# Kernel optimization log

Hardware: AMD Instinct MI355X
Metric: run time of the kernel (lower is better)

The kernel has to match this reference:

```python
import jax, jax.numpy as jnp
import numpy as np

QBITS = 8  # fake-quant bit width from q_config
DT_RANK = 128
D_STATE = 16


def fake_quant_tensor(x, bits=QBITS):
    """Per-tensor symmetric fake quantization (quantize-dequantize) with STE."""
    qmax = 2.0 ** (bits - 1) - 1.0
    s = jnp.maximum(jnp.max(jnp.abs(x)) / qmax, 1e-8)
    q = jnp.clip(jnp.round(x / s), -qmax - 1.0, qmax) * s
    return x + jax.lax.stop_gradient(q - x)


def fake_quant_per_channel(w, bits=QBITS):
    """Per-output-channel symmetric fake quantization for weights [out, in]."""
    qmax = 2.0 ** (bits - 1) - 1.0
    s = jnp.maximum(jnp.max(jnp.abs(w), axis=-1, keepdims=True) / qmax, 1e-8)
    q = jnp.clip(jnp.round(w / s), -qmax - 1.0, qmax) * s
    return w + jax.lax.stop_gradient(q - w)


def setup_inputs() -> dict:
    key = jax.random.key(0)
    ks = jax.random.split(key, 8)
    B, L, D_MODEL = 2, 4096, 2048
    d_inner = D_MODEL  # expand = 1.0
    x = jax.random.normal(ks[0], (B, L, D_MODEL), jnp.float32)
    prompt = 0.1 * jax.random.normal(ks[1], (B, L, D_STATE), jnp.float32)
    # x_proj: Linear(d_inner -> dt_rank + 2*d_state), no bias
    Wx = jax.random.normal(ks[2], (DT_RANK + 2 * D_STATE, d_inner), jnp.float32) / np.sqrt(d_inner)
    # dt_proj: Linear(dt_rank -> d_inner), with bias
    Wdt = jax.random.normal(ks[3], (d_inner, DT_RANK), jnp.float32) / np.sqrt(DT_RANK)
    bdt = 0.1 * jax.random.normal(ks[4], (d_inner,), jnp.float32)
    # S4D-real init for A_log, D skip param (standard Mamba selective-scan params)
    A_log = jnp.log(jnp.tile(jnp.arange(1, D_STATE + 1, dtype=jnp.float32), (d_inner, 1)))
    Dskip = jax.random.normal(ks[5], (d_inner,), jnp.float32)
    return dict(x=x, prompt=prompt, Wx=Wx, Wdt=Wdt, bdt=bdt, A_log=A_log, Dskip=Dskip)


def reference(x, prompt, Wx, Wdt, bdt, A_log, Dskip):
    # x_proj with fake-quantized weight, then split into dt / B / C
    x_dbl = jnp.einsum('bld,od->blo', x, fake_quant_per_channel(Wx))
    dts = x_dbl[..., :DT_RANK]
    Bs = x_dbl[..., DT_RANK:DT_RANK + D_STATE]
    Cs = x_dbl[..., DT_RANK + D_STATE:]
    # dt_proj with fake-quantized weight
    dts = jnp.einsum('blr,or->blo', dts, fake_quant_per_channel(Wdt)) + bdt
    # activation fake-quant of scan inputs
    u_q = fake_quant_tensor(x)          # [B, L, d_inner]
    dt_q = fake_quant_tensor(dts)       # [B, L, d_inner]
    B_q = fake_quant_tensor(Bs)         # [B, L, d_state]
    C_q = fake_quant_tensor(Cs + prompt)  # [B, L, d_state]
    # selective scan (quantized SSM weights A, D)
    A = -jnp.exp(fake_quant_per_channel(A_log))  # [d_inner, d_state]
    D_q = fake_quant_tensor(Dskip)               # [d_inner]
    dt = jax.nn.softplus(dt_q)

    def step(h, inp):
        u_t, dt_t, B_t, C_t = inp  # [B,d], [B,d], [B,n], [B,n]
        dA = jnp.exp(dt_t[:, :, None] * A)             # [B, d, n]
        dBu = (dt_t * u_t)[:, :, None] * B_t[:, None, :]
        h = dA * h + dBu                               # [B, d, n]
        y = jnp.einsum('bdn,bn->bd', h, C_t)
        return h, y

    Bsz, L, d = x.shape
    h0 = jnp.zeros((Bsz, d, D_STATE), x.dtype)
    xs = (jnp.swapaxes(u_q, 0, 1), jnp.swapaxes(dt, 0, 1),
          jnp.swapaxes(B_q, 0, 1), jnp.swapaxes(C_q, 0, 1))
    _, ys = jax.lax.scan(step, h0, xs)  # ys: [L, B, d]
    return jnp.swapaxes(ys, 0, 1) + u_q * D_q
```

## Files before the change

### kernel.cpp

```cpp
#include <hip/hip_runtime.h>
#include <hip/hip_bf16.h>

#define BSZ    2
#define LSEQ   4096
#define DMODEL 2048
#define DTR    128
#define DST    16
#define ODIM   160
#define MROWS  (BSZ*LSEQ)
#define CH     64
#define TT     (LSEQ/CH)
#define STRD   258
#define LOG2E  1.44269504088896340736f
#define LN2    0.69314718055994530942f

typedef short  short8  __attribute__((ext_vector_type(8)));
typedef float  floatx4 __attribute__((ext_vector_type(4)));
typedef float  floatx2 __attribute__((ext_vector_type(2)));

__device__ __forceinline__ unsigned short f2bf(float f) {
    unsigned u = __float_as_uint(f);
    u += 0x7fffu + ((u >> 16) & 1u);
    return (unsigned short)(u >> 16);
}
__device__ __forceinline__ float quantv(float x, float s, float inv_s) {
    float q = rintf(x * inv_s);
    q = fminf(fmaxf(q, -128.0f), 127.0f);
    return q * s;
}
__device__ __forceinline__ float softplus_fast(float v) {
    float t = __builtin_amdgcn_exp2f(-fabsf(v) * LOG2E);
    return fmaxf(v, 0.0f) + LN2 * __log2f(1.0f + t);
}
__device__ __forceinline__ float scale_from_bits(unsigned bits) {
    return fmaxf(__uint_as_float(bits) * (1.0f/127.0f), 1e-8f);
}
__device__ __forceinline__ int pidx(int r, int k, int K) {
    return (r >> 4)*(16*K) + ((k >> 5) << 9) + (((r & 15) + (((k & 31) >> 3) << 4)) << 3) + (k & 7);
}

#define PB_WX  160
#define PB_WDT 128
#define PB_A   128
#define PB_D   1
#define PREP_BLOCKS (PB_WX + PB_WDT + PB_A + PB_D)

__global__ __launch_bounds__(256) void k_prep(
    const float* __restrict__ Wx, const float* __restrict__ Wdt,
    const float* __restrict__ A_log, const float* __restrict__ Dskip,
    unsigned short* __restrict__ Wxq, unsigned short* __restrict__ Wdtq,
    float* __restrict__ a2, float* __restrict__ Dq)
{
    int bid = blockIdx.x, tid = threadIdx.x;
    __shared__ float red[256];
    if (bid < PB_WX) {
        int o = bid, base = o * DMODEL;
        float m = 0.0f;
        for (int i = tid; i < DMODEL; i += 256) m = fmaxf(m, fabsf(Wx[base+i]));
        red[tid] = m; __syncthreads();
        for (int s2 = 128; s2 > 0; s2 >>= 1) { if (tid < s2) red[tid] = fmaxf(red[tid], red[tid+s2]); __syncthreads(); }
        float s = fmaxf(red[0]*(1.0f/127.0f), 1e-8f), inv = 1.0f/s;
        for (int i = tid; i < DMODEL; i += 256)
            Wxq[pidx(o, i, DMODEL)] = f2bf(quantv(Wx[base+i], s, inv));
    } else if (bid < PB_WX + PB_WDT) {
        int n = (bid - PB_WX)*16 + (tid >> 4);
        int k0 = (tid & 15)*8;
        const float* src = Wdt + (size_t)n*DTR + k0;
        float4 v0 = *reinterpret_cast<const float4*>(src);
        float4 v1 = *reinterpret_cast<const float4*>(src + 4);
        float m = fmaxf(fmaxf(fmaxf(fabsf(v0.x), fabsf(v0.y)), fmaxf(fabsf(v0.z), fabsf(v0.w))),
                        fmaxf(fmaxf(fabsf(v1.x), fabsf(v1.y)), fmaxf(fabsf(v1.z), fabsf(v1.w))));
        for (int off = 1; off < 16; off <<= 1) m = fmaxf(m, __shfl_xor(m, off, 16));
        float s = fmaxf(m*(1.0f/127.0f), 1e-8f), inv = 1.0f/s;
        short8 o8;
        o8[0]=(short)f2bf(quantv(v0.x,s,inv)); o8[1]=(short)f2bf(quantv(v0.y,s,inv));
        o8[2]=(short)f2bf(quantv(v0.z,s,inv)); o8[3]=(short)f2bf(quantv(v0.w,s,inv));
        o8[4]=(short)f2bf(quantv(v1.x,s,inv)); o8[5]=(short)f2bf(quantv(v1.y,s,inv));
        o8[6]=(short)f2bf(quantv(v1.z,s,inv)); o8[7]=(short)f2bf(quantv(v1.w,s,inv));
        *reinterpret_cast<short8*>(Wdtq + pidx(n, k0, DTR)) = o8;
    } else if (bid < PB_WX + PB_WDT + PB_A) {
        int d = (bid - PB_WX - PB_WDT)*16 + (tid >> 4);
        int n = tid & 15;
        float v = A_log[d*DST + n];
        float m = fabsf(v);
        for (int off = 1; off < 16; off <<= 1) m = fmaxf(m, __shfl_xor(m, off, 16));
        float s = fmaxf(m*(1.0f/127.0f), 1e-8f);
        float q = quantv(v, s, 1.0f/s);
        a2[d*DST + n] = -expf(q) * LOG2E;
    } else {
        float m = 0.0f;
        for (int i = tid; i < DMODEL; i += 256) m = fmaxf(m, fabsf(Dskip[i]));
        red[tid] = m; __syncthreads();
        for (int s2 = 128; s2 > 0; s2 >>= 1) { if (tid < s2) red[tid] = fmaxf(red[tid], red[tid+s2]); __syncthreads(); }
        float s = fmaxf(red[0]*(1.0f/127.0f), 1e-8f), inv = 1.0f/s;
        for (int i = tid; i < DMODEL; i += 256) Dq[i] = quantv(Dskip[i], s, inv);
    }
}

__global__ __launch_bounds__(256) void k_mm1(
    const float* __restrict__ x, const unsigned short* __restrict__ Wxq,
    const unsigned short* __restrict__ Wdtq, const float* __restrict__ bdt,
    const float* __restrict__ prompt,
    unsigned short* __restrict__ xdblbf, float* __restrict__ xbc,
    unsigned* __restrict__ scales)
{
    int tid = threadIdx.x, w = tid >> 6, lane = tid & 63;
    int mrow = lane & 15, quad = lane >> 4;
    int mt = blockIdx.x, m0 = mt*16, k0 = w*512;
    floatx4 acc[10] = {};
    float xmax = 0.0f;
    const float* arow = x + (size_t)(m0 + mrow)*DMODEL + k0 + quad*8;
    for (int kk = 0; kk < 512; kk += 32) {
        const float4* ap = reinterpret_cast<const float4*>(arow + kk);
        float4 a0 = ap[0], a1 = ap[1];
        xmax = fmaxf(xmax, fmaxf(fmaxf(fabsf(a0.x), fabsf(a0.y)), fmaxf(fabsf(a0.z), fabsf(a0.w))));
        xmax = fmaxf(xmax, fmaxf(fmaxf(fabsf(a1.x), fabsf(a1.y)), fmaxf(fabsf(a1.z), fabsf(a1.w))));
        short8 af;
        af[0]=(short)f2bf(a0.x); af[1]=(short)f2bf(a0.y); af[2]=(short)f2bf(a0.z); af[3]=(short)f2bf(a0.w);
        af[4]=(short)f2bf(a1.x); af[5]=(short)f2bf(a1.y); af[6]=(short)f2bf(a1.z); af[7]=(short)f2bf(a1.w);
        int kcidx = (k0 + kk) >> 5;
        #pragma unroll
        for (int j = 0; j < 10; ++j) {
            short8 bf = *reinterpret_cast<const short8*>(Wxq + j*16*DMODEL + kcidx*512 + lane*8);
            acc[j] = __builtin_amdgcn_mfma_f32_16x16x32_bf16(af, bf, acc[j], 0, 0, 0);
        }
    }
    for (int off = 32; off; off >>= 1) xmax = fmaxf(xmax, __shfl_xor(xmax, off, 64));
    __shared__ float red[4*2560];
    __shared__ float redB[256], redC[256];
    __shared__ float wred[4], wd[4];
    __shared__ unsigned short lds_abf[2048];
    if (lane == 0) wred[w] = xmax;
    #pragma unroll
    for (int j = 0; j < 10; ++j) {
        float4 v = make_float4(acc[j][0], acc[j][1], acc[j][2], acc[j][3]);
        *reinterpret_cast<float4*>(&red[w*2560 + (j*16 + mrow)*16 + quad*4]) = v;
    }
    __syncthreads();
    float bmax = 0.0f, cmax = 0.0f;
    #pragma unroll
    for (int j = 0; j < 10; ++j) {
        int e = j*256 + tid;
        float v = red[e] + red[2560+e] + red[5120+e] + red[7680+e];
        int col = e >> 4, rowin = e & 15, row = m0 + rowin;
        if (col < DTR) {
            int off = ((col>>5)<<9) + ((rowin + (((col&31)>>3)<<4))<<3) + (col&7);
            unsigned short bfb = f2bf(v);
            xdblbf[mt*16*DTR + off] = bfb;
            lds_abf[off] = bfb;
        } else if (col < DTR + DST) {
            bmax = fmaxf(bmax, fabsf(v));
            xbc[(size_t)row*32 + (col - DTR)] = v;
        } else {
            v += prompt[(size_t)row*DST + (col - DTR - DST)];
            cmax = fmaxf(cmax, fabsf(v));
            xbc[(size_t)row*32 + 16 + (col - DTR - DST)] = v;
        }
    }
    redB[tid] = bmax; redC[tid] = cmax; __syncthreads();
    for (int s2 = 128; s2 > 0; s2 >>= 1) {
        if (tid < s2) { redB[tid] = fmaxf(redB[tid], redB[tid+s2]); redC[tid] = fmaxf(redC[tid], redC[tid+s2]); }
        __syncthreads();
    }
    short8 afr[4];
    #pragma unroll
    for (int kc = 0; kc < 4; ++kc)
        afr[kc] = *reinterpret_cast<const short8*>(lds_abf + (kc<<9) + lane*8);
    float dmax = 0.0f;
    for (int jj = 0; jj < 32; ++jj) {
        int ntile = w*32 + jj;
        const unsigned short* bb = Wdtq + (size_t)ntile*16*DTR + lane*8;
        floatx4 acc2 = {};
        #pragma unroll
        for (int kc = 0; kc < 4; ++kc) {
            short8 bf = *reinterpret_cast<const short8*>(bb + (kc<<9));
            acc2 = __builtin_amdgcn_mfma_f32_16x16x32_bf16(afr[kc], bf, acc2, 0, 0, 0);
        }
        float bv = bdt[ntile*16 + mrow];
        #pragma unroll
        for (int r = 0; r < 4; ++r) dmax = fmaxf(dmax, fabsf(acc2[r] + bv));
    }
    for (int off = 32; off; off >>= 1) dmax = fmaxf(dmax, __shfl_xor(dmax, off, 64));
    if (lane == 0) wd[w] = dmax;
    __syncthreads();
    if (tid == 0) {
        atomicMax(&scales[0], __float_as_uint(fmaxf(fmaxf(wred[0], wred[1]), fmaxf(wred[2], wred[3]))));
        atomicMax(&scales[1], __float_as_uint(redB[0]));
        atomicMax(&scales[2], __float_as_uint(redC[0]));
        atomicMax(&scales[3], __float_as_uint(fmaxf(fmaxf(wd[0], wd[1]), fmaxf(wd[2], wd[3]))));
    }
}

__global__ __launch_bounds__(256) void k_scan1(
    const unsigned short* __restrict__ Ap, const unsigned short* __restrict__ Bp,
    const float* __restrict__ bdt, const float* __restrict__ x,
    const float* __restrict__ xbc, const float* __restrict__ a2,
    const unsigned* __restrict__ scales, unsigned* __restrict__ u8g,
    float* __restrict__ Aprod, float* __restrict__ hfin)
{
    int bid = blockIdx.x, tid = threadIdx.x;
    int w = tid >> 6, lane = tid & 63;
    int mrow = lane & 15, quad = lane >> 4;
    int b = bid >> 9, rem = bid & 511, dblk = rem >> 6, ch = rem & 63;
    int d0 = dblk*256, t0 = ch*TT;
    int d = d0 + tid;
    float s_u  = scale_from_bits(scales[0]), inv_su = 1.0f/s_u;
    float s_B  = scale_from_bits(scales[1]), inv_sB  = 1.0f/s_B;
    float s_dt = scale_from_bits(scales[3]), inv_sdt = 1.0f/s_dt;
    floatx2 a22[8];
    {
        const floatx2* ap = reinterpret_cast<const floatx2*>(a2 + (size_t)d*DST);
        #pragma unroll
        for (int i = 0; i < 8; ++i) a22[i] = ap[i];
    }
    floatx2 h2[8];
    #pragma unroll
    for (int i = 0; i < 8; ++i) h2[i] = (floatx2){0.0f, 0.0f};
    float sdt = 0.0f;
    __shared__ float lds_dts[16*STRD];
    __shared__ unsigned lds_u[16*64];
    __shared__ __align__(16) float Bq_p[16*16];
    for (int st = 0; st < TT/16; ++st) {
        int tb = t0 + st*16;
        int gm = (b*LSEQ + tb) >> 4;
        short8 afr[4];
        #pragma unroll
        for (int kc = 0; kc < 4; ++kc)
            afr[kc] = *reinterpret_cast<const short8*>(Ap + (size_t)gm*16*DTR + (kc<<9) + lane*8);
        #pragma unroll
        for (int j = 0; j < 4; ++j) {
            int ntile = dblk*16 + w*4 + j;
            int dloc = w*64 + j*16 + mrow;
            float bdtv = bdt[d0 + dloc];
            floatx4 acc = {};
            #pragma unroll
            for (int kc = 0; kc < 4; ++kc) {
                short8 bf = *reinterpret_cast<const short8*>(Bp + (size_t)ntile*16*DTR + (kc<<9) + lane*8);
                acc = __builtin_amdgcn_mfma_f32_16x16x32_bf16(afr[kc], bf, acc, 0, 0, 0);
            }
            #pragma unroll
            for (int r = 0; r < 4; ++r)
                lds_dts[(quad*4 + r)*STRD + dloc] = acc[r] + bdtv;
        }
        {
            const float4* x4 = reinterpret_cast<const float4*>(x);
            #pragma unroll
            for (int i = 0; i < 4; ++i) {
                int q = i*256 + tid, row = q >> 6, c4 = q & 63;
                size_t gi = (size_t)(b*LSEQ + tb + row)*(DMODEL/4) + dblk*64 + c4;
                float4 v = x4[gi];
                int q0 = (int)fminf(fmaxf(rintf(v.x*inv_su), -128.0f), 127.0f);
                int q1 = (int)fminf(fmaxf(rintf(v.y*inv_su), -128.0f), 127.0f);
                int q2 = (int)fminf(fmaxf(rintf(v.z*inv_su), -128.0f), 127.0f);
                int q3 = (int)fminf(fmaxf(rintf(v.w*inv_su), -128.0f), 127.0f);
                unsigned u = (q0 & 255) | ((q1 & 255) << 8) | ((q2 & 255) << 16) | ((unsigned)(q3 & 255) << 24);
                lds_u[row*64 + c4] = u;
                u8g[gi] = u;
            }
            Bq_p[tid] = quantv(xbc[(size_t)(b*LSEQ + tb + (tid>>4))*32 + (tid&15)], s_B, inv_sB);
        }
        __syncthreads();
        const signed char* lub = reinterpret_cast<const signed char*>(lds_u);
        for (int t = 0; t < 16; ++t) {
            float dtq = quantv(lds_dts[t*STRD + tid], s_dt, inv_sdt);
            float dtv = softplus_fast(dtq);
            float uq  = s_u * (float)lub[t*256 + tid];
            float dtu = dtv * uq;
            sdt += dtv;
            floatx2 dtv2 = {dtv, dtv}, dtu2 = {dtu, dtu};
            const floatx2* bq2 = reinterpret_cast<const floatx2*>(&Bq_p[t*16]);
            #pragma unroll
            for (int n2 = 0; n2 < 8; ++n2) {
                floatx2 e = a22[n2] * dtv2;
                floatx2 dA; dA.x = __builtin_amdgcn_exp2f(e.x); dA.y = __builtin_amdgcn_exp2f(e.y);
                h2[n2] = dA*h2[n2] + bq2[n2]*dtu2;
            }
        }
        __syncthreads();
    }
    size_t ob = ((size_t)((b*CH + ch)*DMODEL + d))*DST;
    floatx2 sdt2 = {sdt, sdt};
    #pragma unroll
    for (int i = 0; i < 4; ++i) {
        floatx2 e0 = a22[2*i] * sdt2, e1 = a22[2*i+1] * sdt2;
        float4 av = make_float4(__builtin_amdgcn_exp2f(e0.x), __builtin_amdgcn_exp2f(e0.y),
                                __builtin_amdgcn_exp2f(e1.x), __builtin_amdgcn_exp2f(e1.y));
        float4 hv = make_float4(h2[2*i].x, h2[2*i].y, h2[2*i+1].x, h2[2*i+1].y);
        *reinterpret_cast<float4*>(Aprod + ob + 4*i) = av;
        *reinterpret_cast<float4*>(hfin  + ob + 4*i) = hv;
    }
}

__global__ __launch_bounds__(256) void k_mid(
    float* __restrict__ Aprod, const float* __restrict__ hfin)
{
    int f = blockIdx.x*256 + threadIdx.x;
    int b = f >> 15, dn = f & 32767;
    size_t base = (size_t)b*CH*32768 + dn;
    float h = 0.0f;
    #pragma unroll 4
    for (int ch = 0; ch < CH; ++ch) {
        size_t o = base + (size_t)ch*32768;
        float a = Aprod[o], hf = hfin[o];
        Aprod[o] = h;
        h = fmaf(a, h, hf);
    }
}

__global__ __launch_bounds__(256) void k_scan3(
    const unsigned short* __restrict__ Ap, const unsigned short* __restrict__ Bp,
    const float* __restrict__ bdt, const unsigned* __restrict__ u8g,
    const float* __restrict__ xbc, const float* __restrict__ a2,
    const float* __restrict__ Dq, const unsigned* __restrict__ scales,
    const float* __restrict__ hinit, float* __restrict__ out)
{
    int bid = blockIdx.x, tid = threadIdx.x;
    int w = tid >> 6, lane = tid & 63;
    int mrow = lane & 15, quad = lane >> 4;
    int b = bid >> 9, rem = bid & 511, dblk = rem >> 6, ch = rem & 63;
    int d0 = dblk*256, t0 = ch*TT;
    int d = d0 + tid;
    float s_u  = scale_from_bits(scales[0]);
    float s_B  = scale_from_bits(scales[1]), inv_sB  = 1.0f/s_B;
    float s_C  = scale_from_bits(scales[2]), inv_sC  = 1.0f/s_C;
    float s_dt = scale_from_bits(scales[3]), inv_sdt = 1.0f/s_dt;
    float dqd = Dq[d];
    floatx2 a22[8];
    {
        const floatx2* ap = reinterpret_cast<const floatx2*>(a2 + (size_t)d*DST);
        #pragma unroll
        for (int i = 0; i < 8; ++i) a22[i] = ap[i];
    }
    size_t ob = ((size_t)((b*CH + ch)*DMODEL + d))*DST;
    floatx2 h2[8];
    #pragma unroll
    for (int i = 0; i < 4; ++i) {
        float4 hv = *reinterpret_cast<const float4*>(hinit + ob + 4*i);
        h2[2*i]   = (floatx2){hv.x, hv.y};
        h2[2*i+1] = (floatx2){hv.z, hv.w};
    }
    __shared__ float lds_dts[16*STRD];
    __shared__ unsigned lds_u[16*64];
    __shared__ __align__(16) float Bq_p[16*16];
    __shared__ __align__(16) float Cq_p[16*16];
    for (int st = 0; st < TT/16; ++st) {
        int tb = t0 + st*16;
        int gm = (b*LSEQ + tb) >> 4;
        short8 afr[4];
        #pragma unroll
        for (int kc = 0; kc < 4; ++kc)
            afr[kc] = *reinterpret_cast<const short8*>(Ap + (size_t)gm*16*DTR + (kc<<9) + lane*8);
        #pragma unroll
        for (int j = 0; j < 4; ++j) {
            int ntile = dblk*16 + w*4 + j;
            int dloc = w*64 + j*16 + mrow;
            float bdtv = bdt[d0 + dloc];
            floatx4 acc = {};
            #pragma unroll
            for (int kc = 0; kc < 4; ++kc) {
                short8 bf = *reinterpret_cast<const short8*>(Bp + (size_t)ntile*16*DTR + (kc<<9) + lane*8);
                acc = __builtin_amdgcn_mfma_f32_16x16x32_bf16(afr[kc], bf, acc, 0, 0, 0);
            }
            #pragma unroll
            for (int r = 0; r < 4; ++r)
                lds_dts[(quad*4 + r)*STRD + dloc] = acc[r] + bdtv;
        }
        {
            #pragma unroll
            for (int i = 0; i < 4; ++i) {
                int q = i*256 + tid, row = q >> 6, c4 = q & 63;
                size_t gi = (size_t)(b*LSEQ + tb + row)*(DMODEL/4) + dblk*64 + c4;
                lds_u[row*64 + c4] = u8g[gi];
            }
            size_t px = (size_t)(b*LSEQ + tb + (tid>>4))*32;
            Bq_p[tid] = quantv(xbc[px + (tid&15)],      s_B, inv_sB);
            Cq_p[tid] = quantv(xbc[px + 16 + (tid&15)], s_C, inv_sC);
        }
        __syncthreads();
        const signed char* lub = reinterpret_cast<const signed char*>(lds_u);
        for (int t = 0; t < 16; ++t) {
            float dtq = quantv(lds_dts[t*STRD + tid], s_dt, inv_sdt);
            float dtv = softplus_fast(dtq);
            float uq  = s_u * (float)lub[t*256 + tid];
            float dtu = dtv * uq;
            floatx2 dtv2 = {dtv, dtv}, dtu2 = {dtu, dtu};
            const floatx2* bq2 = reinterpret_cast<const floatx2*>(&Bq_p[t*16]);
            const floatx2* cq2 = reinterpret_cast<const floatx2*>(&Cq_p[t*16]);
            floatx2 y2 = {0.0f, 0.0f};
            #pragma unroll
            for (int n2 = 0; n2 < 8; ++n2) {
                floatx2 e = a22[n2] * dtv2;
                floatx2 dA; dA.x = __builtin_amdgcn_exp2f(e.x); dA.y = __builtin_amdgcn_exp2f(e.y);
                h2[n2] = dA*h2[n2] + bq2[n2]*dtu2;
                y2 = y2 + h2[n2]*cq2[n2];
            }
            float y = y2.x + y2.y;
            __builtin_nontemporal_store(y + uq * dqd, out + (size_t)(b*LSEQ + tb + t)*DMODEL + d);
        }
        __syncthreads();
    }
}

extern "C" void kernel_launch(void* const* d_in, const int* in_sizes, int n_in,
                              void* d_out, int out_size, void* d_ws, size_t ws_size,
                              hipStream_t stream)
{
    const float* x      = (const float*)d_in[0];
    const float* prompt = (const float*)d_in[1];
    const float* Wx     = (const float*)d_in[2];
    const float* Wdt    = (const float*)d_in[3];
    const float* bdt    = (const float*)d_in[4];
    const float* A_log  = (const float*)d_in[5];
    const float* Dskip  = (const float*)d_in[6];
    float* out = (float*)d_out;
    char* ws = (char*)d_ws;
    size_t off = 0;
    unsigned* scales       = (unsigned*)(ws + off);        off += 256;
    unsigned short* Wxq    = (unsigned short*)(ws + off);  off += (size_t)ODIM*DMODEL*2;
    unsigned short* Wdtq   = (unsigned short*)(ws + off);  off += (size_t)DMODEL*DTR*2;
    float* a2              = (float*)(ws + off);           off += (size_t)DMODEL*DST*4;
    float* Dq              = (float*)(ws + off);           off += (size_t)DMODEL*4;
    float* xbc             = (float*)(ws + off);           off += (size_t)MROWS*32*4;
    unsigned short* xdblbf = (unsigned short*)(ws + off);  off += (size_t)MROWS*DTR*2;
    unsigned* u8g          = (unsigned*)(ws + off);        off += (size_t)MROWS*DMODEL;
    float* Aprod           = (float*)(ws + off);           off += (size_t)BSZ*CH*DMODEL*DST*4;
    float* hfin            = (float*)(ws + off);           off += (size_t)BSZ*CH*DMODEL*DST*4;

    hipMemsetAsync(scales, 0, 256, stream);
    hipLaunchKernelGGL(k_prep, dim3(PREP_BLOCKS), dim3(256), 0, stream,
                       Wx, Wdt, A_log, Dskip, Wxq, Wdtq, a2, Dq);
    hipLaunchKernelGGL(k_mm1, dim3(MROWS/16), dim3(256), 0, stream,
                       x, Wxq, Wdtq, bdt, prompt, xdblbf, xbc, scales);
    hipLaunchKernelGGL(k_scan1, dim3(BSZ*8*CH), dim3(256), 0, stream,
                       xdblbf, Wdtq, bdt, x, xbc, a2, scales, u8g, Aprod, hfin);
    hipLaunchKernelGGL(k_mid, dim3(BSZ*DMODEL*DST/256), dim3(256), 0, stream,
                       Aprod, hfin);
    hipLaunchKernelGGL(k_scan3, dim3(BSZ*8*CH), dim3(256), 0, stream,
                       xdblbf, Wdtq, bdt, u8g, xbc, a2, Dq, scales, Aprod, out);
}
```

Baseline: 328.3 us.

## Store int8 dt codes in scan1, reuse in scan3, double-buffer LDS stages

k_scan1 now quantizes the dt projection to int8 codes and writes them to global memory, so k_scan3 reads them back instead of redoing the dt_proj MFMA matmul. Both scan kernels move to 128-thread blocks with twice as many blocks, and they double-buffer the LDS staging so loads for the next 16-step tile are issued before the current tile's recurrence runs, with one barrier per stage. This removes duplicated matmul work and a barrier per stage. The cost is an extra 16 MB write and read of dt codes and smaller blocks that now stage less data each.

```diff
diff --git a/kernel.cpp b/kernel.cpp
--- a/kernel.cpp
+++ b/kernel.cpp
@@ -10,7 +10,6 @@
 #define MROWS  (BSZ*LSEQ)
 #define CH     64
 #define TT     (LSEQ/CH)
-#define STRD   258
 #define LOG2E  1.44269504088896340736f
 #define LN2    0.69314718055994530942f
 
@@ -27,6 +26,9 @@
     float q = rintf(x * inv_s);
     q = fminf(fmaxf(q, -128.0f), 127.0f);
     return q * s;
+}
+__device__ __forceinline__ int qcode(float x, float inv_s) {
+    return (int)fminf(fmaxf(rintf(x * inv_s), -128.0f), 127.0f);
 }
 __device__ __forceinline__ float softplus_fast(float v) {
     float t = __builtin_amdgcn_exp2f(-fabsf(v) * LOG2E);
@@ -191,18 +193,19 @@
     }
 }
 
-__global__ __launch_bounds__(256) void k_scan1(
+__global__ __launch_bounds__(128) void k_scan1(
     const unsigned short* __restrict__ Ap, const unsigned short* __restrict__ Bp,
     const float* __restrict__ bdt, const float* __restrict__ x,
     const float* __restrict__ xbc, const float* __restrict__ a2,
-    const unsigned* __restrict__ scales, unsigned* __restrict__ u8g,
+    const unsigned* __restrict__ scales,
+    unsigned* __restrict__ u8g, signed char* __restrict__ dt8g,
     float* __restrict__ Aprod, float* __restrict__ hfin)
 {
     int bid = blockIdx.x, tid = threadIdx.x;
     int w = tid >> 6, lane = tid & 63;
     int mrow = lane & 15, quad = lane >> 4;
-    int b = bid >> 9, rem = bid & 511, dblk = rem >> 6, ch = rem & 63;
-    int d0 = dblk*256, t0 = ch*TT;
+    int b = bid >> 10, rem = bid & 1023, dblk = rem >> 6, ch = rem & 63;
+    int d0 = dblk*128, t0 = ch*TT;
     int d = d0 + tid;
     float s_u  = scale_from_bits(scales[0]), inv_su = 1.0f/s_u;
     float s_B  = scale_from_bits(scales[1]), inv_sB  = 1.0f/s_B;
@@ -217,66 +220,75 @@
     #pragma unroll
     for (int i = 0; i < 8; ++i) h2[i] = (floatx2){0.0f, 0.0f};
     float sdt = 0.0f;
-    __shared__ float lds_dts[16*STRD];
-    __shared__ unsigned lds_u[16*64];
-    __shared__ __align__(16) float Bq_p[16*16];
-    for (int st = 0; st < TT/16; ++st) {
-        int tb = t0 + st*16;
-        int gm = (b*LSEQ + tb) >> 4;
-        short8 afr[4];
-        #pragma unroll
-        for (int kc = 0; kc < 4; ++kc)
-            afr[kc] = *reinterpret_cast<const short8*>(Ap + (size_t)gm*16*DTR + (kc<<9) + lane*8);
-        #pragma unroll
-        for (int j = 0; j < 4; ++j) {
-            int ntile = dblk*16 + w*4 + j;
-            int dloc = w*64 + j*16 + mrow;
-            float bdtv = bdt[d0 + dloc];
-            floatx4 acc = {};
+    __shared__ signed char lds_dt8[2][16*128];
+    __shared__ unsigned    lds_u[2][16*32];
+    __shared__ float       lds_B[2][16*16];
+
+    #pragma unroll 1
+    for (int pst = 0; pst <= TT/16; ++pst) {
+        if (pst > 0) __syncthreads();
+        if (pst < TT/16) {
+            int buf = pst & 1;
+            int tb = t0 + pst*16;
+            int gm = (b*LSEQ + tb) >> 4;
+            short8 afr[4];
             #pragma unroll
-            for (int kc = 0; kc < 4; ++kc) {
-                short8 bf = *reinterpret_cast<const short8*>(Bp + (size_t)ntile*16*DTR + (kc<<9) + lane*8);
-                acc = __builtin_amdgcn_mfma_f32_16x16x32_bf16(afr[kc], bf, acc, 0, 0, 0);
+            for (int kc = 0; kc < 4; ++kc)
+                afr[kc] = *reinterpret_cast<const short8*>(Ap + (size_t)gm*16*DTR + (kc<<9) + lane*8);
+            #pragma unroll
+            for (int j = 0; j < 4; ++j) {
+                int ntile = dblk*8 + w*4 + j;
+                int dloc = w*64 + j*16 + mrow;
+                float bdtv = bdt[d0 + dloc];
+                floatx4 acc = {};
+                #pragma unroll
+                for (int kc = 0; kc < 4; ++kc) {
+                    short8 bf = *reinterpret_cast<const short8*>(Bp + (size_t)ntile*16*DTR + (kc<<9) + lane*8);
+                    acc = __builtin_amdgcn_mfma_f32_16x16x32_bf16(afr[kc], bf, acc, 0, 0, 0);
+                }
+                #pragma unroll
+                for (int r = 0; r < 4; ++r) {
+                    signed char c = (signed char)qcode(acc[r] + bdtv, inv_sdt);
+                    lds_dt8[buf][(quad*4 + r)*128 + dloc] = c;
+                    dt8g[(size_t)(b*LSEQ + tb + quad*4 + r)*DMODEL + d0 + dloc] = c;
+                }
             }
-            #pragma unroll
-            for (int r = 0; r < 4; ++r)
-                lds_dts[(quad*4 + r)*STRD + dloc] = acc[r] + bdtv;
-        }
-        {
             const float4* x4 = reinterpret_cast<const float4*>(x);
             #pragma unroll
             for (int i = 0; i < 4; ++i) {
-                int q = i*256 + tid, row = q >> 6, c4 = q & 63;
-                size_t gi = (size_t)(b*LSEQ + tb + row)*(DMODEL/4) + dblk*64 + c4;
+                int q = i*128 + tid, row = q >> 5, c4 = q & 31;
+                size_t gi = (size_t)(b*LSEQ + tb + row)*(DMODEL/4) + dblk*32 + c4;
                 float4 v = x4[gi];
-                int q0 = (int)fminf(fmaxf(rintf(v.x*inv_su), -128.0f), 127.0f);
-                int q1 = (int)fminf(fmaxf(rintf(v.y*inv_su), -128.0f), 127.0f);
-                int q2 = (int)fminf(fmaxf(rintf(v.z*inv_su), -128.0f), 127.0f);
-                int q3 = (int)fminf(fmaxf(rintf(v.w*inv_su), -128.0f), 127.0f);
+                int q0 = qcode(v.x, inv_su), q1 = qcode(v.y, inv_su);
+                int q2 = qcode(v.z, inv_su), q3 = qcode(v.w, inv_su);
                 unsigned u = (q0 & 255) | ((q1 & 255) << 8) | ((q2 & 255) << 16) | ((unsigned)(q3 & 255) << 24);
-                lds_u[row*64 + c4] = u;
+                lds_u[buf][row*32 + c4] = u;
                 u8g[gi] = u;
             }
-            Bq_p[tid] = quantv(xbc[(size_t)(b*LSEQ + tb + (tid>>4))*32 + (tid&15)], s_B, inv_sB);
-        }
-        __syncthreads();
-        const signed char* lub = reinterpret_cast<const signed char*>(lds_u);
-        for (int t = 0; t < 16; ++t) {
-            float dtq = quantv(lds_dts[t*STRD + tid], s_dt, inv_sdt);
-            float dtv = softplus_fast(dtq);
-            float uq  = s_u * (float)lub[t*256 + tid];
-            float dtu = dtv * uq;
-            sdt += dtv;
-            floatx2 dtv2 = {dtv, dtv}, dtu2 = {dtu, dtu};
-            const floatx2* bq2 = reinterpret_cast<const floatx2*>(&Bq_p[t*16]);
-            #pragma unroll
-            for (int n2 = 0; n2 < 8; ++n2) {
-                floatx2 e = a22[n2] * dtv2;
-                floatx2 dA; dA.x = __builtin_amdgcn_exp2f(e.x); dA.y = __builtin_amdgcn_exp2f(e.y);
-                h2[n2] = dA*h2[n2] + bq2[n2]*dtu2;
+            lds_B[buf][tid]       = quantv(xbc[(size_t)(b*LSEQ + tb + (tid>>4))*32 + (tid&15)], s_B, inv_sB);
+            lds_B[buf][tid + 128] = quantv(xbc[(size_t)(b*LSEQ + tb + 8 + (tid>>4))*32 + (tid&15)], s_B, inv_sB);
+        }
+        if (pst > 0) {
+            int buf = (pst - 1) & 1;
+            const signed char* ldt = lds_dt8[buf];
+            const signed char* lub = reinterpret_cast<const signed char*>(lds_u[buf]);
+            const float* lB = lds_B[buf];
+            for (int t = 0; t < 16; ++t) {
+                float dtq = s_dt * (float)ldt[t*128 + tid];
+                float dtv = softplus_fast(dtq);
+                float uq  = s_u * (float)lub[t*128 + tid];
+                float dtu = dtv * uq;
+                sdt += dtv;
+                floatx2 dtv2 = {dtv, dtv}, dtu2 = {dtu, dtu};
+                const floatx2* bq2 = reinterpret_cast<const floatx2*>(lB + t*16);
+                #pragma unroll
+                for (int n2 = 0; n2 < 8; ++n2) {
+                    floatx2 e = a22[n2] * dtv2;
+                    floatx2 dA; dA.x = __builtin_amdgcn_exp2f(e.x); dA.y = __builtin_amdgcn_exp2f(e.y);
+                    h2[n2] = dA*h2[n2] + bq2[n2]*dtu2;
+                }
             }
         }
-        __syncthreads();
     }
     size_t ob = ((size_t)((b*CH + ch)*DMODEL + d))*DST;
     floatx2 sdt2 = {sdt, sdt};
@@ -307,23 +319,20 @@
     }
 }
 
-__global__ __launch_bounds__(256) void k_scan3(
-    const unsigned short* __restrict__ Ap, const unsigned short* __restrict__ Bp,
-    const float* __restrict__ bdt, const unsigned* __restrict__ u8g,
+__global__ __launch_bounds__(128) void k_scan3(
+    const unsigned* __restrict__ u8g, const unsigned* __restrict__ dt8g,
     const float* __restrict__ xbc, const float* __restrict__ a2,
     const float* __restrict__ Dq, const unsigned* __restrict__ scales,
     const float* __restrict__ hinit, float* __restrict__ out)
 {
     int bid = blockIdx.x, tid = threadIdx.x;
-    int w = tid >> 6, lane = tid & 63;
-    int mrow = lane & 15, quad = lane >> 4;
-    int b = bid >> 9, rem = bid & 511, dblk = rem >> 6, ch = rem & 63;
-    int d0 = dblk*256, t0 = ch*TT;
+    int b = bid >> 10, rem = bid & 1023, dblk = rem >> 6, ch = rem & 63;
+    int d0 = dblk*128, t0 = ch*TT;
     int d = d0 + tid;
     float s_u  = scale_from_bits(scales[0]);
     float s_B  = scale_from_bits(scales[1]), inv_sB  = 1.0f/s_B;
     float s_C  = scale_from_bits(scales[2]), inv_sC  = 1.0f/s_C;
-    float s_dt = scale_from_bits(scales[3]), inv_sdt = 1.0f/s_dt;
+    float s_dt = scale_from_bits(scales[3]);
     float dqd = Dq[d];
     floatx2 a22[8];
     {
@@ -339,65 +348,58 @@
         h2[2*i]   = (floatx2){hv.x, hv.y};
         h2[2*i+1] = (floatx2){hv.z, hv.w};
     }
-    __shared__ float lds_dts[16*STRD];
-    __shared__ unsigned lds_u[16*64];
-    __shared__ __align__(16) float Bq_p[16*16];
-    __shared__ __align__(16) float Cq_p[16*16];
-    for (int st = 0; st < TT/16; ++st) {
-        int tb = t0 + st*16;
-        int gm = (b*LSEQ + tb) >> 4;
-        short8 afr[4];
-        #pragma unroll
-        for (int kc = 0; kc < 4; ++kc)
-            afr[kc] = *reinterpret_cast<const short8*>(Ap + (size_t)gm*16*DTR + (kc<<9) + lane*8);
-        #pragma unroll
-        for (int j = 0; j < 4; ++j) {
-            int ntile = dblk*16 + w*4 + j;
-            int dloc = w*64 + j*16 + mrow;
-            float bdtv = bdt[d0 + dloc];
-            floatx4 acc = {};
-            #pragma unroll
-            for (int kc = 0; kc < 4; ++kc) {
-                short8 bf = *reinterpret_cast<const short8*>(Bp + (size_t)ntile*16*DTR + (kc<<9) + lane*8);
-                acc = __builtin_amdgcn_mfma_f32_16x16x32_bf16(afr[kc], bf, acc, 0, 0, 0);
-            }
-            #pragma unroll
-            for (int r = 0; r < 4; ++r)
-                lds_dts[(quad*4 + r)*STRD + dloc] = acc[r] + bdtv;
-        }
-        {
+    __shared__ unsigned lds_dt[2][16*32];
+    __shared__ unsigned lds_u[2][16*32];
+    __shared__ float    lds_B[2][16*16];
+    __shared__ float    lds_C[2][16*16];
+
+    #pragma unroll 1
+    for (int pst = 0; pst <= TT/16; ++pst) {
+        if (pst > 0) __syncthreads();
+        if (pst < TT/16) {
+            int buf = pst & 1;
+            int tb = t0 + pst*16;
             #pragma unroll
             for (int i = 0; i < 4; ++i) {
-                int q = i*256 + tid, row = q >> 6, c4 = q & 63;
-                size_t gi = (size_t)(b*LSEQ + tb + row)*(DMODEL/4) + dblk*64 + c4;
-                lds_u[row*64 + c4] = u8g[gi];
+                int q = i*128 + tid, row = q >> 5, c4 = q & 31;
+                size_t gi = (size_t)(b*LSEQ + tb + row)*(DMODEL/4) + dblk*32 + c4;
+                lds_u[buf][row*32 + c4]  = u8g[gi];
+                lds_dt[buf][row*32 + c4] = dt8g[gi];
             }
             size_t px = (size_t)(b*LSEQ + tb + (tid>>4))*32;
-            Bq_p[tid] = quantv(xbc[px + (tid&15)],      s_B, inv_sB);
-            Cq_p[tid] = quantv(xbc[px + 16 + (tid&15)], s_C, inv_sC);
-        }
-        __syncthreads();
-        const signed char* lub = reinterpret_cast<const signed char*>(lds_u);
-        for (int t = 0; t < 16; ++t) {
-            float dtq = quantv(lds_dts[t*STRD + tid], s_dt, inv_sdt);
-            float dtv = softplus_fast(dtq);
-            float uq  = s_u * (float)lub[t*256 + tid];
-            float dtu = dtv * uq;
-            floatx2 dtv2 = {dtv, dtv}, dtu2 = {dtu, dtu};
-            const floatx2* bq2 = reinterpret_cast<const floatx2*>(&Bq_p[t*16]);
-            const floatx2* cq2 = reinterpret_cast<const floatx2*>(&Cq_p[t*16]);
-            floatx2 y2 = {0.0f, 0.0f};
-            #pragma unroll
-            for (int n2 = 0; n2 < 8; ++n2) {
-                floatx2 e = a22[n2] * dtv2;
-                floatx2 dA; dA.x = __builtin_amdgcn_exp2f(e.x); dA.y = __builtin_amdgcn_exp2f(e.y);
-                h2[n2] = dA*h2[n2] + bq2[n2]*dtu2;
-                y2 = y2 + h2[n2]*cq2[n2];
+            lds_B[buf][tid]       = quantv(xbc[px + (tid&15)],      s_B, inv_sB);
+            lds_C[buf][tid]       = quantv(xbc[px + 16 + (tid&15)], s_C, inv_sC);
+            px = (size_t)(b*LSEQ + tb + 8 + (tid>>4))*32;
+            lds_B[buf][tid + 128] = quantv(xbc[px + (tid&15)],      s_B, inv_sB);
+            lds_C[buf][tid + 128] = quantv(xbc[px + 16 + (tid&15)], s_C, inv_sC);
+        }
+        if (pst > 0) {
+            int buf = (pst - 1) & 1;
+            int tb = t0 + (pst - 1)*16;
+            const signed char* ldt = reinterpret_cast<const signed char*>(lds_dt[buf]);
+            const signed char* lub = reinterpret_cast<const signed char*>(lds_u[buf]);
+            const float* lB = lds_B[buf];
+            const float* lC = lds_C[buf];
+            for (int t = 0; t < 16; ++t) {
+                float dtq = s_dt * (float)ldt[t*128 + tid];
+                float dtv = softplus_fast(dtq);
+                float uq  = s_u * (float)lub[t*128 + tid];
+                float dtu = dtv * uq;
+                floatx2 dtv2 = {dtv, dtv}, dtu2 = {dtu, dtu};
+                const floatx2* bq2 = reinterpret_cast<const floatx2*>(lB + t*16);
+                const floatx2* cq2 = reinterpret_cast<const floatx2*>(lC + t*16);
+                floatx2 y2 = {0.0f, 0.0f};
+                #pragma unroll
+                for (int n2 = 0; n2 < 8; ++n2) {
+                    floatx2 e = a22[n2] * dtv2;
+                    floatx2 dA; dA.x = __builtin_amdgcn_exp2f(e.x); dA.y = __builtin_amdgcn_exp2f(e.y);
+                    h2[n2] = dA*h2[n2] + bq2[n2]*dtu2;
+                    y2 = y2 + h2[n2]*cq2[n2];
+                }
+                float y = y2.x + y2.y;
+                __builtin_nontemporal_store(y + uq * dqd, out + (size_t)(b*LSEQ + tb + t)*DMODEL + d);
             }
-            float y = y2.x + y2.y;
-            __builtin_nontemporal_store(y + uq * dqd, out + (size_t)(b*LSEQ + tb + t)*DMODEL + d);
-        }
-        __syncthreads();
+        }
     }
 }
 
@@ -423,6 +425,7 @@
     float* xbc             = (float*)(ws + off);           off += (size_t)MROWS*32*4;
     unsigned short* xdblbf = (unsigned short*)(ws + off);  off += (size_t)MROWS*DTR*2;
     unsigned* u8g          = (unsigned*)(ws + off);        off += (size_t)MROWS*DMODEL;
+    signed char* dt8g      = (signed char*)(ws + off);     off += (size_t)MROWS*DMODEL;
     float* Aprod           = (float*)(ws + off);           off += (size_t)BSZ*CH*DMODEL*DST*4;
     float* hfin            = (float*)(ws + off);           off += (size_t)BSZ*CH*DMODEL*DST*4;
 
@@ -431,10 +434,10 @@
                        Wx, Wdt, A_log, Dskip, Wxq, Wdtq, a2, Dq);
     hipLaunchKernelGGL(k_mm1, dim3(MROWS/16), dim3(256), 0, stream,
                        x, Wxq, Wdtq, bdt, prompt, xdblbf, xbc, scales);
-    hipLaunchKernelGGL(k_scan1, dim3(BSZ*8*CH), dim3(256), 0, stream,
-                       xdblbf, Wdtq, bdt, x, xbc, a2, scales, u8g, Aprod, hfin);
+    hipLaunchKernelGGL(k_scan1, dim3(BSZ*16*CH), dim3(128), 0, stream,
+                       xdblbf, Wdtq, bdt, x, xbc, a2, scales, u8g, dt8g, Aprod, hfin);
     hipLaunchKernelGGL(k_mid, dim3(BSZ*DMODEL*DST/256), dim3(256), 0, stream,
                        Aprod, hfin);
-    hipLaunchKernelGGL(k_scan3, dim3(BSZ*8*CH), dim3(256), 0, stream,
-                       xdblbf, Wdtq, bdt, u8g, xbc, a2, Dq, scales, Aprod, out);
-}
+    hipLaunchKernelGGL(k_scan3, dim3(BSZ*16*CH), dim3(128), 0, stream,
+                       u8g, (const unsigned*)dt8g, xbc, a2, Dq, scales, Aprod, out);
+}
```

Result: no change. 329.0 us (+0.2%).
